# Performance work log

Hardware: AMD Instinct MI355X
Metric: run time of the kernel (lower is better)

The kernel has to match this reference:

```python
import jax, jax.numpy as jnp
import numpy as np
from jax import lax

H = 512      # hidden_dim
P = 11       # num_patches
T = 200      # patch_size
STRIDE = 180 # patch_stride
L = 2000     # output_length
C = 8        # num_target_channels
B = 1024


def _conv1d(x, w, b, pad):
    # x: (B, Cin, L), w: (Cout, Cin, K) torch OIH layout
    y = lax.conv_general_dilated(x, w, window_strides=(1,), padding=[(pad, pad)],
                                 dimension_numbers=('NCH', 'OIH', 'NCH'))
    return y + b[None, :, None]


def _window():
    fade = min(T // 4, 50)
    w = jnp.ones((T,), dtype=jnp.float32)
    ramp = jnp.linspace(0.0, 1.0, fade, dtype=jnp.float32)
    w = w.at[:fade].set(ramp)
    w = w.at[T - fade:].set(ramp[::-1])
    return w


def setup_inputs() -> dict:
    key = jax.random.key(0)
    ks = jax.random.split(key, 16)
    s = 0.02
    return {
        'expanded_embeddings': jax.random.normal(ks[0], (B, P, C, H), dtype=jnp.float32),
        # patch_decoder: Linear(H,H) -> GELU -> (Dropout eval=identity) -> Linear(H,T)
        'W1': jax.random.normal(ks[1], (H, H), dtype=jnp.float32) * s,
        'b1': jnp.zeros((H,), dtype=jnp.float32),
        'W2': jax.random.normal(ks[2], (H, T), dtype=jnp.float32) * s,
        'b2': jnp.zeros((T,), dtype=jnp.float32),
        # refinement: Conv1d(C,4C,15,p7) GELU Conv1d(4C,2C,15,p7) GELU Conv1d(2C,C,15,p7)
        'rw1': jax.random.normal(ks[3], (4 * C, C, 15), dtype=jnp.float32) * s,
        'rb1': jnp.zeros((4 * C,), dtype=jnp.float32),
        'rw2': jax.random.normal(ks[4], (2 * C, 4 * C, 15), dtype=jnp.float32) * s,
        'rb2': jnp.zeros((2 * C,), dtype=jnp.float32),
        'rw3': jax.random.normal(ks[5], (C, 2 * C, 15), dtype=jnp.float32) * s,
        'rb3': jnp.zeros((C,), dtype=jnp.float32),
        # output_proj: Conv1d(C,C,1)
        'pw': jax.random.normal(ks[6], (C, C, 1), dtype=jnp.float32) * s,
        'pb': jnp.zeros((C,), dtype=jnp.float32),
    }


def reference(expanded_embeddings, W1, b1, W2, b2, rw1, rb1, rw2, rb2, rw3, rb3, pw, pb):
    gelu = lambda x: jax.nn.gelu(x, approximate=False)  # torch default GELU (erf)
    # per-patch MLP decode: (B,P,C,H) -> (B,P,C,T)
    h = gelu(jnp.einsum('bpch,hd->bpcd', expanded_embeddings, W1) + b1)
    patches = jnp.einsum('bpch,ht->bpct', h, W2) + b2

    # overlap-add with triangular-faded window
    win = _window()  # (T,)
    out = jnp.zeros((B, C, L), dtype=jnp.float32)
    wsum = jnp.zeros((L,), dtype=jnp.float32)  # identical across B,C
    for i in range(P):  # small static loop over patches
        s0 = i * STRIDE
        if s0 + T <= L:
            out = out.at[:, :, s0:s0 + T].add(patches[:, i] * win)
            wsum = wsum.at[s0:s0 + T].add(win)
    rec = out / jnp.clip(wsum, 1e-8)[None, None, :]

    # conv refinement + residual
    r = gelu(_conv1d(rec, rw1, rb1, 7))
    r = gelu(_conv1d(r, rw2, rb2, 7))
    r = _conv1d(r, rw3, rb3, 7)
    rec = rec + r
    return _conv1d(rec, pw, pb, 0)
```

## Files before the change

kernel.cpp:

```cpp
#include <hip/hip_runtime.h>
#include <stdint.h>
#include <stddef.h>

#define HD 512
#define NP 11
#define PT 200
#define PSTRIDE 180
#define OL 2000
#define NC 8
#define NB 1024

typedef __bf16 bf16x8 __attribute__((ext_vector_type(8)));
typedef float floatx4 __attribute__((ext_vector_type(4)));

__device__ __forceinline__ unsigned short f2bf(float f) {
    unsigned int u = __float_as_uint(f);
    u = u + 0x7FFFu + ((u >> 16) & 1u);
    return (unsigned short)(u >> 16);
}
__device__ __forceinline__ float bf2f(unsigned short s) {
    return __uint_as_float(((unsigned int)s) << 16);
}
__device__ __forceinline__ float gelu_erf(float x) {
    return 0.5f * x * (1.0f + erff(x * 0.70710678118654752440f));
}
__device__ __forceinline__ void async16(const unsigned short* g, unsigned short* l) {
    __builtin_amdgcn_global_load_lds(
        (const __attribute__((address_space(1))) unsigned int*)g,
        (__attribute__((address_space(3))) unsigned int*)l, 16, 0, 0);
}

__global__ __launch_bounds__(256) void cast_x_kernel(const float* __restrict__ x,
                                                     unsigned short* __restrict__ xb) {
    int idx = blockIdx.x * 256 + threadIdx.x;
    float4 v = ((const float4*)x)[idx];
    ushort4 o;
    o.x = f2bf(v.x); o.y = f2bf(v.y); o.z = f2bf(v.z); o.w = f2bf(v.w);
    ((ushort4*)xb)[idx] = o;
}

__global__ __launch_bounds__(256) void prep_w_kernel(const float* __restrict__ W1,
                                                     const float* __restrict__ W2,
                                                     unsigned short* __restrict__ W1t,
                                                     unsigned short* __restrict__ W2t) {
    int idx = blockIdx.x * 256 + threadIdx.x;
    if (idx < 512 * 512) {
        int n = idx >> 9, k = idx & 511;
        W1t[idx] = f2bf(W1[k * 512 + n]);
    } else {
        int j = idx - 512 * 512;
        int n = j >> 9, k = j & 511;
        W2t[j] = (n < PT) ? f2bf(W2[k * PT + n]) : (unsigned short)0;
    }
}

__global__ __launch_bounds__(256) void prep_cw_kernel(const float* __restrict__ rw1,
                                                      const float* __restrict__ rw2,
                                                      const float* __restrict__ rw3,
                                                      unsigned short* __restrict__ Wt1,
                                                      unsigned short* __restrict__ Wt2,
                                                      unsigned short* __restrict__ Wt3) {
    int idx = blockIdx.x * 256 + threadIdx.x;
    if (idx < 4096) {
        int kb = idx >> 10, rem = idx & 1023, oc = rem >> 5, k = rem & 31;
        int tl = k >> 3, ic = k & 7, tap = kb * 4 + tl;
        Wt1[idx] = (tap < 15) ? f2bf(rw1[(oc * 8 + ic) * 15 + tap]) : (unsigned short)0;
    } else if (idx < 4096 + 7680) {
        int j = idx - 4096;
        int t = j >> 9, rem = j & 511, oc = rem >> 5, ic = rem & 31;
        Wt2[j] = f2bf(rw2[(oc * 32 + ic) * 15 + t]);
    } else {
        int j = idx - 11776;
        int kb = j >> 9, rem = j & 511, m = rem >> 5, k = rem & 31;
        int tl = k >> 4, ic = k & 15, tap = kb * 2 + tl;
        Wt3[j] = (m < 8 && tap < 15) ? f2bf(rw3[(m * 16 + ic) * 15 + tap]) : (unsigned short)0;
    }
}

template<bool FUSE_GELU, bool OUT_BF16, int LOG2_NT>
__global__ __launch_bounds__(256) void gemm_lds_kernel(const unsigned short* __restrict__ A,
                                                       const unsigned short* __restrict__ Bt,
                                                       const float* __restrict__ bias,
                                                       void* __restrict__ Cout,
                                                       int out_stride, int n_valid) {
    __shared__ __align__(16) unsigned short As[128 * 32];
    __shared__ __align__(16) unsigned short Bs[128 * 32];
    const int tid  = threadIdx.x;
    const int lane = tid & 63;
    const int wid  = tid >> 6;
    const int bid  = blockIdx.x;
    const int nt   = (bid >> 3) & ((1 << LOG2_NT) - 1);
    const int mt   = (bid >> (3 + LOG2_NT)) * 8 + (bid & 7);
    const int m0 = mt * 128;
    const int n0 = nt * 128;
    const int mw = (wid >> 1) * 64;
    const int nw = (wid & 1) * 64;
    const int l15  = lane & 15;
    const int quad = lane >> 4;
    const int srow = lane >> 2;
    const int scol = (lane & 3) * 8;

    floatx4 acc[4][4];
#pragma unroll
    for (int i = 0; i < 4; ++i)
#pragma unroll
        for (int j = 0; j < 4; ++j) acc[i][j] = (floatx4)0.0f;

    for (int k0 = 0; k0 < 512; k0 += 32) {
#pragma unroll
        for (int p = 0; p < 2; ++p) {
            const int rbase = wid * 32 + p * 16;
            async16(A  + (size_t)(m0 + rbase + srow) * 512 + k0 + scol, As + rbase * 32);
            async16(Bt + (size_t)(n0 + rbase + srow) * 512 + k0 + scol, Bs + rbase * 32);
        }
        __syncthreads();
        bf16x8 af[4], bfr[4];
#pragma unroll
        for (int t = 0; t < 4; ++t) {
            af[t]  = *(const bf16x8*)(As + (mw + t * 16 + l15) * 32 + quad * 8);
            bfr[t] = *(const bf16x8*)(Bs + (nw + t * 16 + l15) * 32 + quad * 8);
        }
#pragma unroll
        for (int mtl = 0; mtl < 4; ++mtl)
#pragma unroll
            for (int ntl = 0; ntl < 4; ++ntl)
                acc[mtl][ntl] = __builtin_amdgcn_mfma_f32_16x16x32_bf16(af[mtl], bfr[ntl], acc[mtl][ntl], 0, 0, 0);
        __syncthreads();
    }

#pragma unroll
    for (int mtl = 0; mtl < 4; ++mtl) {
#pragma unroll
        for (int ntl = 0; ntl < 4; ++ntl) {
            const int col  = n0 + nw + ntl * 16 + l15;
            const int rowb = m0 + mw + mtl * 16 + quad * 4;
            const bool colok = (col < n_valid);
            float bv = colok ? bias[col] : 0.0f;
#pragma unroll
            for (int r = 0; r < 4; ++r) {
                float v = acc[mtl][ntl][r] + bv;
                if (FUSE_GELU) v = gelu_erf(v);
                if (colok) {
                    size_t off = (size_t)(rowb + r) * out_stride + col;
                    if (OUT_BF16) ((unsigned short*)Cout)[off] = f2bf(v);
                    else          ((float*)Cout)[off] = v;
                }
            }
        }
    }
}

__global__ __launch_bounds__(256) void oadd_kernel(const unsigned short* __restrict__ patches,
                                                   float* __restrict__ rec) {
    int idx = blockIdx.x * 256 + threadIdx.x;
    int l = idx % OL;
    int b = idx / OL;
    int imin = (l >= PT) ? (l - (PT - PSTRIDE)) / PSTRIDE : 0;
    int imax = l / PSTRIDE; if (imax > NP - 1) imax = NP - 1;
    float acc[8];
#pragma unroll
    for (int c = 0; c < 8; ++c) acc[c] = 0.0f;
    float wsum = 0.0f;
    for (int i = imin; i <= imax; ++i) {
        int t = l - i * PSTRIDE;
        float w = (t < 50) ? t * (1.0f / 49.0f)
                           : ((t >= 150) ? (199 - t) * (1.0f / 49.0f) : 1.0f);
        wsum += w;
        const unsigned short* p = patches + ((size_t)(b * NP + i) * NC) * PT + t;
#pragma unroll
        for (int c = 0; c < 8; ++c) acc[c] += bf2f(p[c * PT]) * w;
    }
    float inv = 1.0f / fmaxf(wsum, 1e-8f);
    float4 v0 = { acc[0] * inv, acc[1] * inv, acc[2] * inv, acc[3] * inv };
    float4 v1 = { acc[4] * inv, acc[5] * inv, acc[6] * inv, acc[7] * inv };
    float* o = rec + (size_t)idx * 8;
    *(float4*)o = v0;
    *(float4*)(o + 4) = v1;
}

__global__ __launch_bounds__(256) void conv1_mfma(const float* __restrict__ rec,
                                                  const unsigned short* __restrict__ Wt1,
                                                  const float* __restrict__ rb1,
                                                  unsigned short* __restrict__ c1) {
    __shared__ __align__(16) unsigned short xs[272 * 8];
    __shared__ __align__(16) unsigned short ys[256 * 40];
    __shared__ float bs[32];
    const int tid = threadIdx.x;
    const int b = blockIdx.y;
    const int seg0 = blockIdx.x * 256;
    const int lane = tid & 63, wid = tid >> 6;
    const int l15 = lane & 15, quad = lane >> 4;

    if (tid < 32) bs[tid] = rb1[tid];
    for (int i = tid; i < 544; i += 256) {
        int row = i >> 1, half = i & 1;
        int p = seg0 - 7 + row;
        float4 v = (p >= 0 && p < OL) ? *(const float4*)(rec + ((size_t)b * OL + p) * 8 + half * 4)
                                      : make_float4(0.f, 0.f, 0.f, 0.f);
        ushort4 o; o.x = f2bf(v.x); o.y = f2bf(v.y); o.z = f2bf(v.z); o.w = f2bf(v.w);
        *(ushort4*)(xs + row * 8 + half * 4) = o;
    }
    bf16x8 wfrag[4][2];
#pragma unroll
    for (int kb = 0; kb < 4; ++kb)
#pragma unroll
        for (int ot = 0; ot < 2; ++ot)
            wfrag[kb][ot] = *(const bf16x8*)(Wt1 + (kb * 32 + ot * 16 + l15) * 32 + quad * 8);
    __syncthreads();

    floatx4 acc[2][4];
#pragma unroll
    for (int ot = 0; ot < 2; ++ot)
#pragma unroll
        for (int u = 0; u < 4; ++u) acc[ot][u] = (floatx4)0.0f;

#pragma unroll
    for (int u = 0; u < 4; ++u) {
        const int posl = wid * 64 + u * 16 + l15;
#pragma unroll
        for (int kb = 0; kb < 4; ++kb) {
            int row = posl + kb * 4 + quad;
            bf16x8 bfrag = *(const bf16x8*)(xs + row * 8);
#pragma unroll
            for (int ot = 0; ot < 2; ++ot)
                acc[ot][u] = __builtin_amdgcn_mfma_f32_16x16x32_bf16(wfrag[kb][ot], bfrag, acc[ot][u], 0, 0, 0);
        }
    }
#pragma unroll
    for (int ot = 0; ot < 2; ++ot)
#pragma unroll
        for (int u = 0; u < 4; ++u) {
            int posl = wid * 64 + u * 16 + l15;
            int oc0 = ot * 16 + quad * 4;
            ushort4 o;
            o.x = f2bf(gelu_erf(acc[ot][u][0] + bs[oc0]));
            o.y = f2bf(gelu_erf(acc[ot][u][1] + bs[oc0 + 1]));
            o.z = f2bf(gelu_erf(acc[ot][u][2] + bs[oc0 + 2]));
            o.w = f2bf(gelu_erf(acc[ot][u][3] + bs[oc0 + 3]));
            *(ushort4*)(ys + posl * 40 + oc0) = o;
        }
    __syncthreads();
    for (int i = tid; i < 1024; i += 256) {
        int row = i >> 2, ch = i & 3;
        int p = seg0 + row;
        if (p < OL)
            *(int4*)(c1 + ((size_t)b * OL + p) * 32 + ch * 8) = *(const int4*)(ys + row * 40 + ch * 8);
    }
}

__global__ __launch_bounds__(256) void conv2_mfma(const unsigned short* __restrict__ c1,
                                                  const unsigned short* __restrict__ Wt2,
                                                  const float* __restrict__ rb2,
                                                  unsigned short* __restrict__ c2) {
    __shared__ __align__(16) unsigned short xs[270 * 40];
    __shared__ __align__(16) unsigned short ys[256 * 24];
    __shared__ float bs[16];
    const int tid = threadIdx.x;
    const int b = blockIdx.y;
    const int seg0 = blockIdx.x * 256;
    const int lane = tid & 63, wid = tid >> 6;
    const int l15 = lane & 15, quad = lane >> 4;

    if (tid < 16) bs[tid] = rb2[tid];
    for (int i = tid; i < 1080; i += 256) {
        int row = i >> 2, ch = i & 3;
        int p = seg0 - 7 + row;
        int4 v = (p >= 0 && p < OL) ? *(const int4*)(c1 + ((size_t)b * OL + p) * 32 + ch * 8)
                                    : make_int4(0, 0, 0, 0);
        *(int4*)(xs + row * 40 + ch * 8) = v;
    }
    bf16x8 wfrag[15];
#pragma unroll
    for (int t = 0; t < 15; ++t)
        wfrag[t] = *(const bf16x8*)(Wt2 + (t * 16 + l15) * 32 + quad * 8);
    __syncthreads();

    floatx4 acc[4];
#pragma unroll
    for (int u = 0; u < 4; ++u) acc[u] = (floatx4)0.0f;

#pragma unroll
    for (int u = 0; u < 4; ++u) {
        const int posl = wid * 64 + u * 16 + l15;
#pragma unroll
        for (int t = 0; t < 15; ++t) {
            bf16x8 bfrag = *(const bf16x8*)(xs + (posl + t) * 40 + quad * 8);
            acc[u] = __builtin_amdgcn_mfma_f32_16x16x32_bf16(wfrag[t], bfrag, acc[u], 0, 0, 0);
        }
    }
#pragma unroll
    for (int u = 0; u < 4; ++u) {
        int posl = wid * 64 + u * 16 + l15;
        int oc0 = quad * 4;
        ushort4 o;
        o.x = f2bf(gelu_erf(acc[u][0] + bs[oc0]));
        o.y = f2bf(gelu_erf(acc[u][1] + bs[oc0 + 1]));
        o.z = f2bf(gelu_erf(acc[u][2] + bs[oc0 + 2]));
        o.w = f2bf(gelu_erf(acc[u][3] + bs[oc0 + 3]));
        *(ushort4*)(ys + posl * 24 + oc0) = o;
    }
    __syncthreads();
    for (int i = tid; i < 512; i += 256) {
        int row = i >> 1, ch = i & 1;
        int p = seg0 + row;
        if (p < OL)
            *(int4*)(c2 + ((size_t)b * OL + p) * 16 + ch * 8) = *(const int4*)(ys + row * 24 + ch * 8);
    }
}

__global__ __launch_bounds__(256) void conv3pw_mfma(const unsigned short* __restrict__ c2,
                                                    const float* __restrict__ rec,
                                                    const unsigned short* __restrict__ Wt3,
                                                    const float* __restrict__ rb3,
                                                    const float* __restrict__ pw,
                                                    const float* __restrict__ pb,
                                                    float* __restrict__ out) {
    __shared__ __align__(16) unsigned short xs[272 * 24];
    __shared__ __align__(16) float r2[256 * 12];
    __shared__ float pws[64], bs3[8], bsp[8];
    const int tid = threadIdx.x;
    const int b = blockIdx.y;
    const int seg0 = blockIdx.x * 256;
    const int lane = tid & 63, wid = tid >> 6;
    const int l15 = lane & 15, quad = lane >> 4;

    if (tid < 64) pws[tid] = pw[tid];
    if (tid >= 64 && tid < 72) bs3[tid - 64] = rb3[tid - 64];
    if (tid >= 72 && tid < 80) bsp[tid - 72] = pb[tid - 72];
    for (int i = tid; i < 544; i += 256) {
        int row = i >> 1, ch = i & 1;
        int p = seg0 - 7 + row;
        int4 v = (p >= 0 && p < OL) ? *(const int4*)(c2 + ((size_t)b * OL + p) * 16 + ch * 8)
                                    : make_int4(0, 0, 0, 0);
        *(int4*)(xs + row * 24 + ch * 8) = v;
    }
    for (int i = tid; i < 512; i += 256) {
        int row = i >> 1, half = i & 1;
        int p = seg0 + row;
        float4 v = (p < OL) ? *(const float4*)(rec + ((size_t)b * OL + p) * 8 + half * 4)
                            : make_float4(0.f, 0.f, 0.f, 0.f);
        *(float4*)(r2 + row * 12 + half * 4) = v;
    }
    bf16x8 wfrag[8];
#pragma unroll
    for (int kb = 0; kb < 8; ++kb)
        wfrag[kb] = *(const bf16x8*)(Wt3 + (kb * 16 + l15) * 32 + quad * 8);
    __syncthreads();

    floatx4 acc[4];
#pragma unroll
    for (int u = 0; u < 4; ++u) acc[u] = (floatx4)0.0f;

#pragma unroll
    for (int u = 0; u < 4; ++u) {
        const int posl = wid * 64 + u * 16 + l15;
#pragma unroll
        for (int kb = 0; kb < 8; ++kb) {
            int row = posl + kb * 2 + (quad >> 1);
            bf16x8 bfrag = *(const bf16x8*)(xs + row * 24 + (quad & 1) * 8);
            acc[u] = __builtin_amdgcn_mfma_f32_16x16x32_bf16(wfrag[kb], bfrag, acc[u], 0, 0, 0);
        }
    }
    if (quad < 2) {
#pragma unroll
        for (int u = 0; u < 4; ++u) {
            int posl = wid * 64 + u * 16 + l15;
            int oc0 = quad * 4;
            float4 rv = *(const float4*)(r2 + posl * 12 + oc0);
            rv.x += acc[u][0] + bs3[oc0];
            rv.y += acc[u][1] + bs3[oc0 + 1];
            rv.z += acc[u][2] + bs3[oc0 + 2];
            rv.w += acc[u][3] + bs3[oc0 + 3];
            *(float4*)(r2 + posl * 12 + oc0) = rv;
        }
    }
    __syncthreads();
    {
        int p = seg0 + tid;
        if (p < OL) {
            float4 a = *(const float4*)(r2 + tid * 12);
            float4 c = *(const float4*)(r2 + tid * 12 + 4);
#pragma unroll
            for (int o = 0; o < 8; ++o) {
                float v = bsp[o];
                v += pws[o * 8 + 0] * a.x + pws[o * 8 + 1] * a.y + pws[o * 8 + 2] * a.z + pws[o * 8 + 3] * a.w;
                v += pws[o * 8 + 4] * c.x + pws[o * 8 + 5] * c.y + pws[o * 8 + 6] * c.z + pws[o * 8 + 7] * c.w;
                out[((size_t)b * 8 + o) * OL + p] = v;
            }
        }
    }
}

extern "C" void kernel_launch(void* const* d_in, const int* in_sizes, int n_in,
                              void* d_out, int out_size, void* d_ws, size_t ws_size,
                              hipStream_t stream) {
    const float* X   = (const float*)d_in[0];
    const float* W1  = (const float*)d_in[1];
    const float* b1  = (const float*)d_in[2];
    const float* W2  = (const float*)d_in[3];
    const float* b2  = (const float*)d_in[4];
    const float* rw1 = (const float*)d_in[5];
    const float* rb1 = (const float*)d_in[6];
    const float* rw2 = (const float*)d_in[7];
    const float* rb2 = (const float*)d_in[8];
    const float* rw3 = (const float*)d_in[9];
    const float* rb3 = (const float*)d_in[10];
    const float* pw  = (const float*)d_in[11];
    const float* pb  = (const float*)d_in[12];
    float* out = (float*)d_out;

    char* ws = (char*)d_ws;
    unsigned short* Xb  = (unsigned short*)(ws);
    unsigned short* W1t = (unsigned short*)(ws +  92274688);
    unsigned short* W2t = (unsigned short*)(ws +  92798976);
    unsigned short* h   = (unsigned short*)(ws +  93061120);
    unsigned short* pat = (unsigned short*)(ws + 185335808);
    float*          rec = (float*)         (ws + 257425408);
    unsigned short* Wt1 = (unsigned short*)(ws + 322961408);
    unsigned short* Wt2 = (unsigned short*)(ws + 322969600);
    unsigned short* Wt3 = (unsigned short*)(ws + 322984960);
    unsigned short* c1  = (unsigned short*)(ws);
    unsigned short* c2  = (unsigned short*)(ws + 131072000);

    cast_x_kernel<<<45056, 256, 0, stream>>>(X, Xb);
    prep_w_kernel<<<1536, 256, 0, stream>>>(W1, W2, W1t, W2t);
    prep_cw_kernel<<<62, 256, 0, stream>>>(rw1, rw2, rw3, Wt1, Wt2, Wt3);
    gemm_lds_kernel<true,  true, 2><<<2816, 256, 0, stream>>>(Xb, W1t, b1, (void*)h,   512, 512);
    gemm_lds_kernel<false, true, 1><<<1408, 256, 0, stream>>>(h,  W2t, b2, (void*)pat, 200, 200);
    oadd_kernel<<<8000, 256, 0, stream>>>(pat, rec);
    conv1_mfma<<<dim3(8, NB), 256, 0, stream>>>(rec, Wt1, rb1, c1);
    conv2_mfma<<<dim3(8, NB), 256, 0, stream>>>(c1, Wt2, rb2, c2);
    conv3pw_mfma<<<dim3(8, NB), 256, 0, stream>>>(c2, rec, Wt3, rb3, pw, pb, out);
}
```

Measured before the change: 607.7 us.

## Fuse overlap-add and three conv stages into one tiled kernel with halo recompute

Replaces the overlap-add kernel and the three separate conv kernels with one kernel per 256-position segment. The reconstruction is computed directly from the bf16 patches, and a 21-position halo is recomputed so each conv stage reads its input from LDS. This removes the global round trips of the fp32 rec buffer and the c1/c2 intermediates, plus three kernel launches. The cost is extra halo work (304 rows for 256 outputs), more LDS per block, which may lower occupancy, and the residual now comes from the fp32 values held in LDS.

After: 572.6 us. 5.8% less time.

```diff
diff --git a/kernel.cpp b/kernel.cpp
--- a/kernel.cpp
+++ b/kernel.cpp
@@ -150,231 +150,167 @@
     }
 }
 
-__global__ __launch_bounds__(256) void oadd_kernel(const unsigned short* __restrict__ patches,
-                                                   float* __restrict__ rec) {
-    int idx = blockIdx.x * 256 + threadIdx.x;
-    int l = idx % OL;
-    int b = idx / OL;
-    int imin = (l >= PT) ? (l - (PT - PSTRIDE)) / PSTRIDE : 0;
-    int imax = l / PSTRIDE; if (imax > NP - 1) imax = NP - 1;
-    float acc[8];
-#pragma unroll
-    for (int c = 0; c < 8; ++c) acc[c] = 0.0f;
-    float wsum = 0.0f;
-    for (int i = imin; i <= imax; ++i) {
-        int t = l - i * PSTRIDE;
-        float w = (t < 50) ? t * (1.0f / 49.0f)
-                           : ((t >= 150) ? (199 - t) * (1.0f / 49.0f) : 1.0f);
-        wsum += w;
-        const unsigned short* p = patches + ((size_t)(b * NP + i) * NC) * PT + t;
-#pragma unroll
-        for (int c = 0; c < 8; ++c) acc[c] += bf2f(p[c * PT]) * w;
-    }
-    float inv = 1.0f / fmaxf(wsum, 1e-8f);
-    float4 v0 = { acc[0] * inv, acc[1] * inv, acc[2] * inv, acc[3] * inv };
-    float4 v1 = { acc[4] * inv, acc[5] * inv, acc[6] * inv, acc[7] * inv };
-    float* o = rec + (size_t)idx * 8;
-    *(float4*)o = v0;
-    *(float4*)(o + 4) = v1;
-}
-
-__global__ __launch_bounds__(256) void conv1_mfma(const float* __restrict__ rec,
+__global__ __launch_bounds__(256) void tail_fused(const unsigned short* __restrict__ pat,
                                                   const unsigned short* __restrict__ Wt1,
                                                   const float* __restrict__ rb1,
-                                                  unsigned short* __restrict__ c1) {
-    __shared__ __align__(16) unsigned short xs[272 * 8];
-    __shared__ __align__(16) unsigned short ys[256 * 40];
-    __shared__ float bs[32];
+                                                  const unsigned short* __restrict__ Wt2,
+                                                  const float* __restrict__ rb2,
+                                                  const unsigned short* __restrict__ Wt3,
+                                                  const float* __restrict__ rb3,
+                                                  const float* __restrict__ pw,
+                                                  const float* __restrict__ pb,
+                                                  float* __restrict__ out) {
+    __shared__ __align__(16) unsigned short xs[304 * 8];
+    __shared__ __align__(16) unsigned short ys1[288 * 40];
+    __shared__ __align__(16) unsigned short ys2[272 * 24];
+    __shared__ __align__(16) float r2[256 * 12];
+    __shared__ float pws[64], bs1[32], bs2[16], bs3[8], bsp[8];
     const int tid = threadIdx.x;
     const int b = blockIdx.y;
     const int seg0 = blockIdx.x * 256;
     const int lane = tid & 63, wid = tid >> 6;
     const int l15 = lane & 15, quad = lane >> 4;
 
-    if (tid < 32) bs[tid] = rb1[tid];
-    for (int i = tid; i < 544; i += 256) {
-        int row = i >> 1, half = i & 1;
-        int p = seg0 - 7 + row;
-        float4 v = (p >= 0 && p < OL) ? *(const float4*)(rec + ((size_t)b * OL + p) * 8 + half * 4)
-                                      : make_float4(0.f, 0.f, 0.f, 0.f);
-        ushort4 o; o.x = f2bf(v.x); o.y = f2bf(v.y); o.z = f2bf(v.z); o.w = f2bf(v.w);
-        *(ushort4*)(xs + row * 8 + half * 4) = o;
-    }
-    bf16x8 wfrag[4][2];
-#pragma unroll
-    for (int kb = 0; kb < 4; ++kb)
-#pragma unroll
-        for (int ot = 0; ot < 2; ++ot)
-            wfrag[kb][ot] = *(const bf16x8*)(Wt1 + (kb * 32 + ot * 16 + l15) * 32 + quad * 8);
+    if (tid < 64) pws[tid] = pw[tid];
+    else if (tid < 96)  bs1[tid - 64]  = rb1[tid - 64];
+    else if (tid < 112) bs2[tid - 96]  = rb2[tid - 96];
+    else if (tid < 120) bs3[tid - 112] = rb3[tid - 112];
+    else if (tid < 128) bsp[tid - 120] = pb[tid - 120];
+
+    for (int row = tid; row < 304; row += 256) {
+        int p = seg0 - 21 + row;
+        float acc[8];
+#pragma unroll
+        for (int c = 0; c < 8; ++c) acc[c] = 0.0f;
+        if (p >= 0 && p < OL) {
+            int imin = (p >= PT) ? (p - (PT - PSTRIDE)) / PSTRIDE : 0;
+            int imax = p / PSTRIDE; if (imax > NP - 1) imax = NP - 1;
+            float wsum = 0.0f;
+            for (int i = imin; i <= imax; ++i) {
+                int t = p - i * PSTRIDE;
+                float w = (t < 50) ? t * (1.0f / 49.0f)
+                                   : ((t >= 150) ? (199 - t) * (1.0f / 49.0f) : 1.0f);
+                wsum += w;
+                const unsigned short* pp = pat + ((size_t)(b * NP + i) * NC) * PT + t;
+#pragma unroll
+                for (int c = 0; c < 8; ++c) acc[c] += bf2f(pp[c * PT]) * w;
+            }
+            float inv = 1.0f / fmaxf(wsum, 1e-8f);
+#pragma unroll
+            for (int c = 0; c < 8; ++c) acc[c] *= inv;
+        }
+        ushort4 o0, o1;
+        o0.x = f2bf(acc[0]); o0.y = f2bf(acc[1]); o0.z = f2bf(acc[2]); o0.w = f2bf(acc[3]);
+        o1.x = f2bf(acc[4]); o1.y = f2bf(acc[5]); o1.z = f2bf(acc[6]); o1.w = f2bf(acc[7]);
+        *(ushort4*)(xs + row * 8)     = o0;
+        *(ushort4*)(xs + row * 8 + 4) = o1;
+        int cr = row - 21;
+        if (cr >= 0 && cr < 256) {
+            float4 v0 = { acc[0], acc[1], acc[2], acc[3] };
+            float4 v1 = { acc[4], acc[5], acc[6], acc[7] };
+            *(float4*)(r2 + cr * 12)     = v0;
+            *(float4*)(r2 + cr * 12 + 4) = v1;
+        }
+    }
     __syncthreads();
 
-    floatx4 acc[2][4];
-#pragma unroll
-    for (int ot = 0; ot < 2; ++ot)
-#pragma unroll
-        for (int u = 0; u < 4; ++u) acc[ot][u] = (floatx4)0.0f;
-
-#pragma unroll
-    for (int u = 0; u < 4; ++u) {
-        const int posl = wid * 64 + u * 16 + l15;
-#pragma unroll
-        for (int kb = 0; kb < 4; ++kb) {
-            int row = posl + kb * 4 + quad;
-            bf16x8 bfrag = *(const bf16x8*)(xs + row * 8);
+    {
+        bf16x8 wf[4][2];
+#pragma unroll
+        for (int kb = 0; kb < 4; ++kb)
 #pragma unroll
             for (int ot = 0; ot < 2; ++ot)
-                acc[ot][u] = __builtin_amdgcn_mfma_f32_16x16x32_bf16(wfrag[kb][ot], bfrag, acc[ot][u], 0, 0, 0);
-        }
-    }
-#pragma unroll
-    for (int ot = 0; ot < 2; ++ot)
-#pragma unroll
-        for (int u = 0; u < 4; ++u) {
-            int posl = wid * 64 + u * 16 + l15;
-            int oc0 = ot * 16 + quad * 4;
-            ushort4 o;
-            o.x = f2bf(gelu_erf(acc[ot][u][0] + bs[oc0]));
-            o.y = f2bf(gelu_erf(acc[ot][u][1] + bs[oc0 + 1]));
-            o.z = f2bf(gelu_erf(acc[ot][u][2] + bs[oc0 + 2]));
-            o.w = f2bf(gelu_erf(acc[ot][u][3] + bs[oc0 + 3]));
-            *(ushort4*)(ys + posl * 40 + oc0) = o;
-        }
+                wf[kb][ot] = *(const bf16x8*)(Wt1 + (kb * 32 + ot * 16 + l15) * 32 + quad * 8);
+#pragma unroll
+        for (int u = 0; u < 5; ++u) {
+            const int base = wid * 80 + u * 16;
+            if (base < 288) {
+                const int posl = base + l15;
+                floatx4 a0 = (floatx4)0.0f, a1 = (floatx4)0.0f;
+#pragma unroll
+                for (int kb = 0; kb < 4; ++kb) {
+                    int row = posl + kb * 4 + quad;
+                    bf16x8 bfrag = *(const bf16x8*)(xs + row * 8);
+                    a0 = __builtin_amdgcn_mfma_f32_16x16x32_bf16(wf[kb][0], bfrag, a0, 0, 0, 0);
+                    a1 = __builtin_amdgcn_mfma_f32_16x16x32_bf16(wf[kb][1], bfrag, a1, 0, 0, 0);
+                }
+                int oc0 = quad * 4;
+                ushort4 o;
+                o.x = f2bf(gelu_erf(a0[0] + bs1[oc0]));
+                o.y = f2bf(gelu_erf(a0[1] + bs1[oc0 + 1]));
+                o.z = f2bf(gelu_erf(a0[2] + bs1[oc0 + 2]));
+                o.w = f2bf(gelu_erf(a0[3] + bs1[oc0 + 3]));
+                *(ushort4*)(ys1 + posl * 40 + oc0) = o;
+                int oc1 = 16 + quad * 4;
+                o.x = f2bf(gelu_erf(a1[0] + bs1[oc1]));
+                o.y = f2bf(gelu_erf(a1[1] + bs1[oc1 + 1]));
+                o.z = f2bf(gelu_erf(a1[2] + bs1[oc1 + 2]));
+                o.w = f2bf(gelu_erf(a1[3] + bs1[oc1 + 3]));
+                *(ushort4*)(ys1 + posl * 40 + oc1) = o;
+            }
+        }
+    }
     __syncthreads();
-    for (int i = tid; i < 1024; i += 256) {
-        int row = i >> 2, ch = i & 3;
-        int p = seg0 + row;
-        if (p < OL)
-            *(int4*)(c1 + ((size_t)b * OL + p) * 32 + ch * 8) = *(const int4*)(ys + row * 40 + ch * 8);
-    }
-}
-
-__global__ __launch_bounds__(256) void conv2_mfma(const unsigned short* __restrict__ c1,
-                                                  const unsigned short* __restrict__ Wt2,
-                                                  const float* __restrict__ rb2,
-                                                  unsigned short* __restrict__ c2) {
-    __shared__ __align__(16) unsigned short xs[270 * 40];
-    __shared__ __align__(16) unsigned short ys[256 * 24];
-    __shared__ float bs[16];
-    const int tid = threadIdx.x;
-    const int b = blockIdx.y;
-    const int seg0 = blockIdx.x * 256;
-    const int lane = tid & 63, wid = tid >> 6;
-    const int l15 = lane & 15, quad = lane >> 4;
-
-    if (tid < 16) bs[tid] = rb2[tid];
-    for (int i = tid; i < 1080; i += 256) {
-        int row = i >> 2, ch = i & 3;
-        int p = seg0 - 7 + row;
-        int4 v = (p >= 0 && p < OL) ? *(const int4*)(c1 + ((size_t)b * OL + p) * 32 + ch * 8)
-                                    : make_int4(0, 0, 0, 0);
-        *(int4*)(xs + row * 40 + ch * 8) = v;
-    }
-    bf16x8 wfrag[15];
-#pragma unroll
-    for (int t = 0; t < 15; ++t)
-        wfrag[t] = *(const bf16x8*)(Wt2 + (t * 16 + l15) * 32 + quad * 8);
+
+    {
+        bf16x8 wf[15];
+#pragma unroll
+        for (int t = 0; t < 15; ++t)
+            wf[t] = *(const bf16x8*)(Wt2 + (t * 16 + l15) * 32 + quad * 8);
+#pragma unroll
+        for (int u = 0; u < 5; ++u) {
+            const int base = wid * 80 + u * 16;
+            if (base < 272) {
+                const int posl = base + l15;
+                floatx4 a = (floatx4)0.0f;
+#pragma unroll
+                for (int t = 0; t < 15; ++t) {
+                    bf16x8 bfrag = *(const bf16x8*)(ys1 + (posl + t) * 40 + quad * 8);
+                    a = __builtin_amdgcn_mfma_f32_16x16x32_bf16(wf[t], bfrag, a, 0, 0, 0);
+                }
+                int oc0 = quad * 4;
+                ushort4 o;
+                o.x = f2bf(gelu_erf(a[0] + bs2[oc0]));
+                o.y = f2bf(gelu_erf(a[1] + bs2[oc0 + 1]));
+                o.z = f2bf(gelu_erf(a[2] + bs2[oc0 + 2]));
+                o.w = f2bf(gelu_erf(a[3] + bs2[oc0 + 3]));
+                *(ushort4*)(ys2 + posl * 24 + oc0) = o;
+            }
+        }
+    }
     __syncthreads();
 
-    floatx4 acc[4];
-#pragma unroll
-    for (int u = 0; u < 4; ++u) acc[u] = (floatx4)0.0f;
-
-#pragma unroll
-    for (int u = 0; u < 4; ++u) {
-        const int posl = wid * 64 + u * 16 + l15;
-#pragma unroll
-        for (int t = 0; t < 15; ++t) {
-            bf16x8 bfrag = *(const bf16x8*)(xs + (posl + t) * 40 + quad * 8);
-            acc[u] = __builtin_amdgcn_mfma_f32_16x16x32_bf16(wfrag[t], bfrag, acc[u], 0, 0, 0);
-        }
-    }
-#pragma unroll
-    for (int u = 0; u < 4; ++u) {
-        int posl = wid * 64 + u * 16 + l15;
-        int oc0 = quad * 4;
-        ushort4 o;
-        o.x = f2bf(gelu_erf(acc[u][0] + bs[oc0]));
-        o.y = f2bf(gelu_erf(acc[u][1] + bs[oc0 + 1]));
-        o.z = f2bf(gelu_erf(acc[u][2] + bs[oc0 + 2]));
-        o.w = f2bf(gelu_erf(acc[u][3] + bs[oc0 + 3]));
-        *(ushort4*)(ys + posl * 24 + oc0) = o;
+    {
+        bf16x8 wf[8];
+#pragma unroll
+        for (int kb = 0; kb < 8; ++kb)
+            wf[kb] = *(const bf16x8*)(Wt3 + (kb * 16 + l15) * 32 + quad * 8);
+#pragma unroll
+        for (int u = 0; u < 5; ++u) {
+            const int base = wid * 80 + u * 16;
+            if (base < 256) {
+                const int posl = base + l15;
+                floatx4 a = (floatx4)0.0f;
+#pragma unroll
+                for (int kb = 0; kb < 8; ++kb) {
+                    int row = posl + kb * 2 + (quad >> 1);
+                    bf16x8 bfrag = *(const bf16x8*)(ys2 + row * 24 + (quad & 1) * 8);
+                    a = __builtin_amdgcn_mfma_f32_16x16x32_bf16(wf[kb], bfrag, a, 0, 0, 0);
+                }
+                if (quad < 2) {
+                    int oc0 = quad * 4;
+                    float4 rv = *(const float4*)(r2 + posl * 12 + oc0);
+                    rv.x += a[0] + bs3[oc0];
+                    rv.y += a[1] + bs3[oc0 + 1];
+                    rv.z += a[2] + bs3[oc0 + 2];
+                    rv.w += a[3] + bs3[oc0 + 3];
+                    *(float4*)(r2 + posl * 12 + oc0) = rv;
+                }
+            }
+        }
     }
     __syncthreads();
-    for (int i = tid; i < 512; i += 256) {
-        int row = i >> 1, ch = i & 1;
-        int p = seg0 + row;
-        if (p < OL)
-            *(int4*)(c2 + ((size_t)b * OL + p) * 16 + ch * 8) = *(const int4*)(ys + row * 24 + ch * 8);
-    }
-}
-
-__global__ __launch_bounds__(256) void conv3pw_mfma(const unsigned short* __restrict__ c2,
-                                                    const float* __restrict__ rec,
-                                                    const unsigned short* __restrict__ Wt3,
-                                                    const float* __restrict__ rb3,
-                                                    const float* __restrict__ pw,
-                                                    const float* __restrict__ pb,
-                                                    float* __restrict__ out) {
-    __shared__ __align__(16) unsigned short xs[272 * 24];
-    __shared__ __align__(16) float r2[256 * 12];
-    __shared__ float pws[64], bs3[8], bsp[8];
-    const int tid = threadIdx.x;
-    const int b = blockIdx.y;
-    const int seg0 = blockIdx.x * 256;
-    const int lane = tid & 63, wid = tid >> 6;
-    const int l15 = lane & 15, quad = lane >> 4;
-
-    if (tid < 64) pws[tid] = pw[tid];
-    if (tid >= 64 && tid < 72) bs3[tid - 64] = rb3[tid - 64];
-    if (tid >= 72 && tid < 80) bsp[tid - 72] = pb[tid - 72];
-    for (int i = tid; i < 544; i += 256) {
-        int row = i >> 1, ch = i & 1;
-        int p = seg0 - 7 + row;
-        int4 v = (p >= 0 && p < OL) ? *(const int4*)(c2 + ((size_t)b * OL + p) * 16 + ch * 8)
-                                    : make_int4(0, 0, 0, 0);
-        *(int4*)(xs + row * 24 + ch * 8) = v;
-    }
-    for (int i = tid; i < 512; i += 256) {
-        int row = i >> 1, half = i & 1;
-        int p = seg0 + row;
-        float4 v = (p < OL) ? *(const float4*)(rec + ((size_t)b * OL + p) * 8 + half * 4)
-                            : make_float4(0.f, 0.f, 0.f, 0.f);
-        *(float4*)(r2 + row * 12 + half * 4) = v;
-    }
-    bf16x8 wfrag[8];
-#pragma unroll
-    for (int kb = 0; kb < 8; ++kb)
-        wfrag[kb] = *(const bf16x8*)(Wt3 + (kb * 16 + l15) * 32 + quad * 8);
-    __syncthreads();
-
-    floatx4 acc[4];
-#pragma unroll
-    for (int u = 0; u < 4; ++u) acc[u] = (floatx4)0.0f;
-
-#pragma unroll
-    for (int u = 0; u < 4; ++u) {
-        const int posl = wid * 64 + u * 16 + l15;
-#pragma unroll
-        for (int kb = 0; kb < 8; ++kb) {
-            int row = posl + kb * 2 + (quad >> 1);
-            bf16x8 bfrag = *(const bf16x8*)(xs + row * 24 + (quad & 1) * 8);
-            acc[u] = __builtin_amdgcn_mfma_f32_16x16x32_bf16(wfrag[kb], bfrag, acc[u], 0, 0, 0);
-        }
-    }
-    if (quad < 2) {
-#pragma unroll
-        for (int u = 0; u < 4; ++u) {
-            int posl = wid * 64 + u * 16 + l15;
-            int oc0 = quad * 4;
-            float4 rv = *(const float4*)(r2 + posl * 12 + oc0);
-            rv.x += acc[u][0] + bs3[oc0];
-            rv.y += acc[u][1] + bs3[oc0 + 1];
-            rv.z += acc[u][2] + bs3[oc0 + 2];
-            rv.w += acc[u][3] + bs3[oc0 + 3];
-            *(float4*)(r2 + posl * 12 + oc0) = rv;
-        }
-    }
-    __syncthreads();
+
     {
         int p = seg0 + tid;
         if (p < OL) {
@@ -415,20 +351,14 @@
     unsigned short* W2t = (unsigned short*)(ws +  92798976);
     unsigned short* h   = (unsigned short*)(ws +  93061120);
     unsigned short* pat = (unsigned short*)(ws + 185335808);
-    float*          rec = (float*)         (ws + 257425408);
     unsigned short* Wt1 = (unsigned short*)(ws + 322961408);
     unsigned short* Wt2 = (unsigned short*)(ws + 322969600);
     unsigned short* Wt3 = (unsigned short*)(ws + 322984960);
-    unsigned short* c1  = (unsigned short*)(ws);
-    unsigned short* c2  = (unsigned short*)(ws + 131072000);
 
     cast_x_kernel<<<45056, 256, 0, stream>>>(X, Xb);
     prep_w_kernel<<<1536, 256, 0, stream>>>(W1, W2, W1t, W2t);
     prep_cw_kernel<<<62, 256, 0, stream>>>(rw1, rw2, rw3, Wt1, Wt2, Wt3);
     gemm_lds_kernel<true,  true, 2><<<2816, 256, 0, stream>>>(Xb, W1t, b1, (void*)h,   512, 512);
     gemm_lds_kernel<false, true, 1><<<1408, 256, 0, stream>>>(h,  W2t, b2, (void*)pat, 200, 200);
-    oadd_kernel<<<8000, 256, 0, stream>>>(pat, rec);
-    conv1_mfma<<<dim3(8, NB), 256, 0, stream>>>(rec, Wt1, rb1, c1);
-    conv2_mfma<<<dim3(8, NB), 256, 0, stream>>>(c1, Wt2, rb2, c2);
-    conv3pw_mfma<<<dim3(8, NB), 256, 0, stream>>>(c2, rec, Wt3, rb3, pw, pb, out);
-}
+    tail_fused<<<dim3(8, NB), 256, 0, stream>>>(pat, Wt1, rb1, Wt2, rb2, Wt3, rb3, pw, pb, out);
+}
```
